# Kernel tuning notes

Hardware: AMD Instinct MI355X
Metric: run time of the kernel (lower is better)

## Reference

```python
import jax, jax.numpy as jnp
import numpy as np

B, S, D = 1, 2048, 2048      # batch, seq, hidden_dim
DF = 768                      # moe intermediate (per routed expert)
DSH = 2048                    # shared-expert intermediate
E, K = 32, 8                  # num routed experts, top_k
BLK = 128                     # fp8 block-scale size
CAP = 1024
T = B * S


def _dequant(w, s, blk=BLK):
    # w: [E, M, N] fp8 values (stored fp32), s: [E, M/blk, N/blk] block scales
    Eh, M, N = w.shape
    Mb, Nb = s.shape[1], s.shape[2]
    return (w.reshape(Eh, Mb, blk, Nb, blk) * s[:, :, None, :, None]).reshape(Eh, M, N)


def setup_inputs() -> dict:
    key = jax.random.key(0)
    ks = jax.random.split(key, 13)
    n = lambda k, shp, sc=0.02: jax.random.normal(k, shp, jnp.float32) * sc
    u = lambda k, shp: jax.random.uniform(k, shp, jnp.float32, 0.005, 0.02)
    return {
        "hidden_states": jax.random.normal(ks[0], (B, S, D), jnp.float32),
        "router_w": n(ks[1], (E, D)),
        # raw fp8-value weights (simulated as fp32 integers-in-range values) + block scale_inv
        "wg_fp8": jax.random.normal(ks[2], (E, DF, D), jnp.float32),
        "sg": u(ks[3], (E, DF // BLK, D // BLK)),
        "wu_fp8": jax.random.normal(ks[4], (E, DF, D), jnp.float32),
        "su": u(ks[5], (E, DF // BLK, D // BLK)),
        "wd_fp8": jax.random.normal(ks[6], (E, D, DF), jnp.float32),
        "sd": u(ks[7], (E, D // BLK, DF // BLK)),
        "ws_gate": n(ks[8], (DSH, D)),
        "ws_up": n(ks[9], (DSH, D)),
        "ws_down": n(ks[10], (D, DSH)),
        "w_shared_gate": n(ks[11], (1, D)),
    }


def reference(hidden_states, router_w, wg_fp8, sg, wu_fp8, su, wd_fp8, sd,
              ws_gate, ws_up, ws_down, w_shared_gate):
    x = hidden_states.reshape(-1, D)  # [T, D]

    # shared expert (SwiGLU) + its sigmoid gate
    shared = (jax.nn.silu(x @ ws_gate.T) * (x @ ws_up.T)) @ ws_down.T
    sh_gate = jax.nn.sigmoid(x @ w_shared_gate.T)  # [T, 1]

    # router: softmax -> top-k -> renormalize (Qwen MoE gate)
    probs = jax.nn.softmax(x @ router_w.T, axis=-1)          # [T, E]
    rw, sel = jax.lax.top_k(probs, K)                        # [T, K]
    rw = rw / jnp.sum(rw, axis=-1, keepdims=True)

    # capacity-based dispatch (replaces the python per-expert loop; same math)
    flat_e = sel.reshape(-1)                                 # [T*K]
    oh = jax.nn.one_hot(flat_e, E, dtype=jnp.int32)
    pos = jnp.sum(jnp.cumsum(oh, axis=0) * oh, axis=-1) - 1  # position within expert
    keep = (pos < CAP)
    pos_c = jnp.minimum(pos, CAP)                            # overflow -> scratch slot CAP
    tok = jnp.arange(T * K) // K                             # owning token of each (t,k) pair

    buf = jnp.zeros((E, CAP + 1, D), x.dtype).at[flat_e, pos_c].set(x[tok])

    # block-scale dequant (fp8*scale_inv), then per-expert SwiGLU
    Wg = _dequant(wg_fp8, sg)
    Wu = _dequant(wu_fp8, su)
    Wd = _dequant(wd_fp8, sd)
    g = jnp.einsum('ecd,efd->ecf', buf, Wg)
    up = jnp.einsum('ecd,efd->ecf', buf, Wu)
    h = jax.nn.silu(g) * up
    y = jnp.einsum('ecf,edf->ecd', h, Wd)                    # [E, CAP+1, D]

    # weighted scatter-add back to tokens (index_add_ equivalent)
    y_tok = y[flat_e, pos_c]                                 # [T*K, D]
    w_tok = rw.reshape(-1) * keep.astype(x.dtype)
    out = jax.ops.segment_sum(y_tok * w_tok[:, None], tok, num_segments=T)

    out = out + sh_gate * shared
    return out.reshape(B, S, D)
```

## Files before the change

kernel.cpp:

```cpp
#include <hip/hip_runtime.h>
#include <hip/hip_bf16.h>


#define TT   2048
#define DD   2048
#define DFF  768
#define DSH  2048
#define EE   32
#define KTOP 8
#define CAP  1024

typedef _Float16 half8  __attribute__((ext_vector_type(8)));
typedef _Float16 half4v __attribute__((ext_vector_type(4)));
typedef float    f32x4  __attribute__((ext_vector_type(4)));

__global__ __launch_bounds__(256) void k_init(int* __restrict__ cnt,
                                              int* __restrict__ slot_tok) {
  int i = blockIdx.x * 256 + threadIdx.x;
  if (i < EE * CAP) slot_tok[i] = 0;
  if (i < EE) cnt[i] = 0;
}

__global__ __launch_bounds__(64) void k_router(
    const float* __restrict__ x, const float* __restrict__ rw,
    const float* __restrict__ wshg,
    _Float16* __restrict__ x_h,
    float* __restrict__ shg, int* __restrict__ cnt,
    int* __restrict__ slot_tok, float* __restrict__ slot_w,
    int* __restrict__ slot_pair, int* __restrict__ pair_pos) {
  int t = blockIdx.x;
  int lane = threadIdx.x;
  const float* xr = x + (size_t)t * DD;
  float xv[32];
#pragma unroll
  for (int j = 0; j < 32; ++j) xv[j] = xr[lane + j * 64];

#pragma unroll
  for (int j = 0; j < 32; ++j)
    x_h[(size_t)t * DD + lane + j * 64] = (_Float16)xv[j];

  __shared__ float lg[EE];
  for (int e = 0; e < EE; ++e) {
    const float* we = rw + (size_t)e * DD;
    float s = 0.f;
#pragma unroll
    for (int j = 0; j < 32; ++j) s += xv[j] * we[lane + j * 64];
#pragma unroll
    for (int off = 32; off > 0; off >>= 1) s += __shfl_down(s, off);
    if (lane == 0) lg[e] = s;
  }
  {
    float s = 0.f;
#pragma unroll
    for (int j = 0; j < 32; ++j) s += xv[j] * wshg[lane + j * 64];
#pragma unroll
    for (int off = 32; off > 0; off >>= 1) s += __shfl_down(s, off);
    if (lane == 0) shg[t] = 1.f / (1.f + expf(-s));
  }
  if (lane == 0) {
    unsigned used = 0;
    int sel[KTOP];
    float val[KTOP];
    for (int k = 0; k < KTOP; ++k) {
      float bv = -1e30f; int bi = 0;
      for (int e = 0; e < EE; ++e)
        if (!((used >> e) & 1) && lg[e] > bv) { bv = lg[e]; bi = e; }
      used |= (1u << bi);
      sel[k] = bi; val[k] = bv;
    }
    float mx = val[0], sum = 0.f;
    for (int k = 0; k < KTOP; ++k) { val[k] = expf(val[k] - mx); sum += val[k]; }
    float inv = 1.f / sum;
    for (int k = 0; k < KTOP; ++k) {
      int e = sel[k];
      int pos = atomicAdd(&cnt[e], 1);
      pair_pos[t * KTOP + k] = pos;
      if (pos < CAP) {
        slot_tok[e * CAP + pos] = t;
        slot_w[e * CAP + pos] = val[k] * inv;
        slot_pair[e * CAP + pos] = t * KTOP + k;
      }
    }
  }
}

template<bool DUAL, bool GATHER, bool DEQ, int EPI, int KDIM>
__device__ __forceinline__ void gemm_body(
    _Float16 (*sA)[8192], _Float16 (*sB)[8192],
    const _Float16* __restrict__ Ae,
    const float* __restrict__ B0e, const float* __restrict__ B1e,
    const float* __restrict__ S0e, const float* __restrict__ S1e, int sRow,
    _Float16* __restrict__ OutH, long long outBase, int ldOut,
    int ldA, int rows, int rowBase, int nBase,
    const int* __restrict__ slotBase, const float* __restrict__ slotW) {
  constexpr int BK = 64;
  constexpr int KT = KDIM / BK;
  constexpr int NF = DUAL ? 2 : 4;
  constexpr int BCH = DUAL ? 4 : 8;

  const int tid = threadIdx.x;
  const int lane = tid & 63;
  const int wave = tid >> 6;
  const int wr = wave >> 1;
  const int wc = wave & 1;

  int aByte[4];
#pragma unroll
  for (int i = 0; i < 4; ++i) {
    int c = tid + i * 256;
    int row = c >> 3;
    int colB = ((c & 7) << 4) ^ ((row & 7) << 4);
    int src = GATHER ? slotBase[rowBase + row] : (rowBase + row);
    aByte[i] = src * (2 * ldA) + colB;
  }
  int bOff[BCH], wByte[BCH];
#pragma unroll
  for (int i = 0; i < BCH; ++i) {
    int c = tid + i * 256;
    int rn = c >> 4;
    int c4 = (c & 15) << 2;
    bOff[i] = (nBase + rn) * KDIM + c4;
    wByte[i] = ((rn << 7) + (c4 << 1)) ^ ((rn & 7) << 4);
  }

  f32x4 accG[4][NF];
  f32x4 accU[DUAL ? 4 : 1][NF];
#pragma unroll
  for (int m = 0; m < 4; ++m)
#pragma unroll
    for (int n = 0; n < NF; ++n) {
      accG[m][n] = (f32x4){0.f, 0.f, 0.f, 0.f};
      if constexpr (DUAL) accU[m][n] = (f32x4){0.f, 0.f, 0.f, 0.f};
    }

  auto stageA = [&](int kt, int buf) {
#pragma unroll
    for (int i = 0; i < 4; ++i) {
      __builtin_amdgcn_global_load_lds(
          (const __attribute__((address_space(1))) void*)
              ((const char*)Ae + aByte[i] + kt * (BK * 2)),
          (__attribute__((address_space(3))) void*)&sA[buf][(tid + i * 256) * 8],
          16, 0, 0);
    }
  };
  auto loadB = [&](int kt, float4 (&r0)[BCH], float4 (&r1)[BCH]) {
    const int ko = kt * BK;
#pragma unroll
    for (int i = 0; i < BCH; ++i) r0[i] = *(const float4*)(B0e + bOff[i] + ko);
    if constexpr (DUAL) {
#pragma unroll
      for (int i = 0; i < BCH; ++i) r1[i] = *(const float4*)(B1e + bOff[i] + ko);
    }
  };
  auto storeB = [&](int kt, float4 (&r0)[BCH], float4 (&r1)[BCH]) {
    float s0 = 1.f, s1 = 1.f;
    if constexpr (DEQ) {
      s0 = S0e[sRow + (kt >> 1)];
      if constexpr (DUAL) s1 = S1e[sRow + (kt >> 1)];
    }
    char* base = (char*)&sB[kt & 1][0];
#pragma unroll
    for (int i = 0; i < BCH; ++i) {
      half4v h = { (_Float16)(r0[i].x * s0), (_Float16)(r0[i].y * s0),
                   (_Float16)(r0[i].z * s0), (_Float16)(r0[i].w * s0) };
      *(half4v*)(base + wByte[i]) = h;
      if constexpr (DUAL) {
        half4v h1 = { (_Float16)(r1[i].x * s1), (_Float16)(r1[i].y * s1),
                      (_Float16)(r1[i].z * s1), (_Float16)(r1[i].w * s1) };
        *(half4v*)(base + 8192 + wByte[i]) = h1;
      }
    }
  };
  auto computeTile = [&](int ia, int ib) {
    const char* pA = (const char*)&sA[ia][0];
    const char* pB = (const char*)&sB[ib][0];
#pragma unroll
    for (int kk = 0; kk < 2; ++kk) {
      const int koff = kk * 32 + (lane >> 4) * 8;
      half8 a[4];
#pragma unroll
      for (int m = 0; m < 4; ++m) {
        int r = wr * 64 + m * 16 + (lane & 15);
        int byt = ((r << 7) + (koff << 1)) ^ ((r & 7) << 4);
        a[m] = *(const half8*)(pA + byt);
      }
      if constexpr (DUAL) {
        half8 bg[2], bu[2];
#pragma unroll
        for (int n = 0; n < 2; ++n) {
          int rn = wc * 32 + n * 16 + (lane & 15);
          int byt = ((rn << 7) + (koff << 1)) ^ ((rn & 7) << 4);
          bg[n] = *(const half8*)(pB + byt);
          bu[n] = *(const half8*)(pB + 8192 + byt);
        }
#pragma unroll
        for (int m = 0; m < 4; ++m)
#pragma unroll
          for (int n = 0; n < 2; ++n) {
            accG[m][n] = __builtin_amdgcn_mfma_f32_16x16x32_f16(a[m], bg[n], accG[m][n], 0, 0, 0);
            accU[m][n] = __builtin_amdgcn_mfma_f32_16x16x32_f16(a[m], bu[n], accU[m][n], 0, 0, 0);
          }
      } else {
        half8 b[4];
#pragma unroll
        for (int n = 0; n < 4; ++n) {
          int rn = wc * 64 + n * 16 + (lane & 15);
          int byt = ((rn << 7) + (koff << 1)) ^ ((rn & 7) << 4);
          b[n] = *(const half8*)(pB + byt);
        }
#pragma unroll
        for (int m = 0; m < 4; ++m)
#pragma unroll
          for (int n = 0; n < 4; ++n)
            accG[m][n] = __builtin_amdgcn_mfma_f32_16x16x32_f16(a[m], b[n], accG[m][n], 0, 0, 0);
      }
    }
  };

  float4 rbE0[BCH], rbE1[BCH], rbO0[BCH], rbO1[BCH];

  stageA(0, 0); loadB(0, rbE0, rbE1);
  __builtin_amdgcn_sched_barrier(0);
  stageA(1, 1); loadB(1, rbO0, rbO1);
  __builtin_amdgcn_sched_barrier(0);

  int bufC = 0;
  int bufW = 2;

  for (int kt = 0; kt < KT; kt += 2) {
    if (kt + 1 < KT) { asm volatile("s_waitcnt vmcnt(12)" ::: "memory"); }
    else             { asm volatile("s_waitcnt vmcnt(0)"  ::: "memory"); }
    __builtin_amdgcn_sched_barrier(0);
    storeB(kt, rbE0, rbE1);
    asm volatile("s_waitcnt lgkmcnt(0)" ::: "memory");
    __builtin_amdgcn_sched_barrier(0);
    __builtin_amdgcn_s_barrier();
    __builtin_amdgcn_sched_barrier(0);
    if (kt + 2 < KT) { stageA(kt + 2, bufW); loadB(kt + 2, rbE0, rbE1); }
    __builtin_amdgcn_sched_barrier(0);
    computeTile(bufC, 0);
    bufC = (bufC == 2) ? 0 : bufC + 1;
    bufW = (bufW == 2) ? 0 : bufW + 1;

    if (kt + 2 < KT) { asm volatile("s_waitcnt vmcnt(12)" ::: "memory"); }
    else             { asm volatile("s_waitcnt vmcnt(0)"  ::: "memory"); }
    __builtin_amdgcn_sched_barrier(0);
    storeB(kt + 1, rbO0, rbO1);
    asm volatile("s_waitcnt lgkmcnt(0)" ::: "memory");
    __builtin_amdgcn_sched_barrier(0);
    __builtin_amdgcn_s_barrier();
    __builtin_amdgcn_sched_barrier(0);
    if (kt + 3 < KT) { stageA(kt + 3, bufW); loadB(kt + 3, rbO0, rbO1); }
    __builtin_amdgcn_sched_barrier(0);
    computeTile(bufC, 1);
    bufC = (bufC == 2) ? 0 : bufC + 1;
    bufW = (bufW == 2) ? 0 : bufW + 1;
  }

#pragma unroll
  for (int m = 0; m < 4; ++m) {
#pragma unroll
    for (int i = 0; i < 4; ++i) {
      int row = rowBase + wr * 64 + m * 16 + (lane >> 4) * 4 + i;
      if (row < rows) {
        if constexpr (EPI == 1) {
          int pair = slotBase[row];
          float w = slotW[row];
#pragma unroll
          for (int n = 0; n < NF; ++n) {
            int col = nBase + wc * 64 + n * 16 + (lane & 15);
            OutH[(long long)pair * DD + col] = (_Float16)(w * accG[m][n][i]);
          }
        } else {
#pragma unroll
          for (int n = 0; n < NF; ++n) {
            int col = nBase + (DUAL ? wc * 32 : wc * 64) + n * 16 + (lane & 15);
            long long o = outBase + (long long)row * ldOut + col;
            if constexpr (DUAL) {
              float gv = accG[m][n][i];
              float uv = accU[m][n][i];
              OutH[o] = (_Float16)((gv / (1.f + __expf(-gv))) * uv);
            } else {
              OutH[o] = (_Float16)accG[m][n][i];
            }
          }
        }
      }
    }
  }
}

__global__ __launch_bounds__(256, 2) void k_gu(
    const _Float16* __restrict__ x_h,
    const float* __restrict__ wg, const float* __restrict__ wu,
    const float* __restrict__ sg, const float* __restrict__ su,
    _Float16* __restrict__ H,
    const float* __restrict__ wsg, const float* __restrict__ wsu,
    _Float16* __restrict__ Hsh,
    const int* __restrict__ cnt, const int* __restrict__ slot_tok) {
  __shared__ __align__(16) _Float16 sA[3][8192];
  __shared__ __align__(16) _Float16 sB[2][8192];
  const int bid = blockIdx.x;
  if (bid < 3072) {
    const int xcd = bid & 7, t0 = bid >> 3;
    const int mb = t0 % 8, pp = t0 / 8;
    const int p = pp * 8 + xcd;
    const int nb = p % 12, e = p / 12;
    int rows = cnt[e] > CAP ? CAP : cnt[e];
    const int rowBase = mb * 128;
    if (rowBase >= rows) return;
    gemm_body<true, true, true, 0, DD>(
        sA, sB, x_h,
        wg + (long long)e * DFF * DD, wu + (long long)e * DFF * DD,
        sg + (long long)e * ((DFF / 128) * (DD / 128)),
        su + (long long)e * ((DFF / 128) * (DD / 128)),
        ((nb * 64) >> 7) * (DD / 128),
        H, (long long)e * CAP * DFF, DFF,
        DD, rows, rowBase, nb * 64,
        slot_tok + e * CAP, nullptr);
  } else {
    const int f = bid - 3072;
    const int xcd = f & 7, t0 = f >> 3;
    const int mb = t0 % 16, pp = t0 / 16;
    const int nb = pp * 8 + xcd;
    gemm_body<true, false, false, 0, DD>(
        sA, sB, x_h,
        wsg, wsu, nullptr, nullptr, 0,
        Hsh, 0LL, DSH,
        DD, TT, mb * 128, nb * 64,
        nullptr, nullptr);
  }
}

__global__ __launch_bounds__(256, 2) void k_dn(
    const _Float16* __restrict__ H,
    const float* __restrict__ wd, const float* __restrict__ sd,
    _Float16* __restrict__ Yp,
    const _Float16* __restrict__ Hsh, const float* __restrict__ wsd,
    _Float16* __restrict__ Ysh,
    const int* __restrict__ cnt,
    const int* __restrict__ slot_pair, const float* __restrict__ slot_w) {
  __shared__ __align__(16) _Float16 sA[3][8192];
  __shared__ __align__(16) _Float16 sB[2][8192];
  const int bid = blockIdx.x;
  if (bid < 4096) {
    const int xcd = bid & 7, t0 = bid >> 3;
    const int mb = t0 % 8, pp = t0 / 8;
    const int p = pp * 8 + xcd;
    const int nb = p % 16, e = p / 16;
    int rows = cnt[e] > CAP ? CAP : cnt[e];
    const int rowBase = mb * 128;
    if (rowBase >= rows) return;
    gemm_body<false, false, true, 1, DFF>(
        sA, sB, H + (long long)e * CAP * DFF,
        wd + (long long)e * DD * DFF, wd + (long long)e * DD * DFF,
        sd + (long long)e * ((DD / 128) * (DFF / 128)), nullptr,
        ((nb * 128) >> 7) * (DFF / 128),
        Yp, 0LL, DD,
        DFF, rows, rowBase, nb * 128,
        slot_pair + e * CAP, slot_w + e * CAP);
  } else {
    const int f = bid - 4096;
    const int xcd = f & 7, t0 = f >> 3;
    const int mb = t0 % 16, pp = t0 / 16;
    const int nb = pp * 8 + xcd;
    gemm_body<false, false, false, 0, DSH>(
        sA, sB, Hsh,
        wsd, wsd, nullptr, nullptr, 0,
        Ysh, 0LL, DD,
        DSH, TT, mb * 128, nb * 128,
        nullptr, nullptr);
  }
}

__global__ __launch_bounds__(256) void k_combine2(
    const _Float16* __restrict__ Yp, const _Float16* __restrict__ Ysh,
    const float* __restrict__ shg, const int* __restrict__ pair_pos,
    float* __restrict__ out) {
  int t = blockIdx.x;
  int col = threadIdx.x * 8;
  float acc[8];
  half8 ys = *(const half8*)&Ysh[(size_t)t * DD + col];
  float g = shg[t];
#pragma unroll
  for (int j = 0; j < 8; ++j) acc[j] = g * (float)ys[j];
#pragma unroll
  for (int k = 0; k < KTOP; ++k) {
    if (pair_pos[t * KTOP + k] < CAP) {
      half8 y = *(const half8*)&Yp[((size_t)t * KTOP + k) * DD + col];
#pragma unroll
      for (int j = 0; j < 8; ++j) acc[j] += (float)y[j];
    }
  }
  float4 o0 = {acc[0], acc[1], acc[2], acc[3]};
  float4 o1 = {acc[4], acc[5], acc[6], acc[7]};
  *(float4*)&out[(size_t)t * DD + col] = o0;
  *(float4*)&out[(size_t)t * DD + col + 4] = o1;
}

extern "C" void kernel_launch(void* const* d_in, const int* in_sizes, int n_in,
                              void* d_out, int out_size, void* d_ws, size_t ws_size,
                              hipStream_t stream) {
  (void)in_sizes; (void)n_in; (void)out_size; (void)ws_size;
  const float* x    = (const float*)d_in[0];
  const float* rw   = (const float*)d_in[1];
  const float* wg   = (const float*)d_in[2];
  const float* sg   = (const float*)d_in[3];
  const float* wu   = (const float*)d_in[4];
  const float* su   = (const float*)d_in[5];
  const float* wd   = (const float*)d_in[6];
  const float* sd   = (const float*)d_in[7];
  const float* wsg  = (const float*)d_in[8];
  const float* wsu  = (const float*)d_in[9];
  const float* wsd  = (const float*)d_in[10];
  const float* wshg = (const float*)d_in[11];
  float* out = (float*)d_out;

  char* p = (char*)d_ws;
  auto alloc = [&](size_t bytes) {
    char* r = p;
    p += (bytes + 255) & ~(size_t)255;
    return r;
  };
  _Float16* x_h   = (_Float16*)alloc((size_t)TT * DD * 2);
  _Float16* H     = (_Float16*)alloc((size_t)EE * CAP * DFF * 2);
  _Float16* Hsh   = (_Float16*)alloc((size_t)TT * DSH * 2);
  _Float16* Yp    = (_Float16*)alloc((size_t)TT * KTOP * DD * 2);
  _Float16* Ysh   = (_Float16*)alloc((size_t)TT * DD * 2);
  float* shg      = (float*)alloc((size_t)TT * 4);
  int* cnt        = (int*)alloc((size_t)EE * 4);
  int* slot_tok   = (int*)alloc((size_t)EE * CAP * 4);
  float* slot_w   = (float*)alloc((size_t)EE * CAP * 4);
  int* slot_pair  = (int*)alloc((size_t)EE * CAP * 4);
  int* pair_pos   = (int*)alloc((size_t)TT * KTOP * 4);

  k_init<<<(EE * CAP + 255) / 256, 256, 0, stream>>>(cnt, slot_tok);
  k_router<<<TT, 64, 0, stream>>>(x, rw, wshg, x_h, shg, cnt, slot_tok,
                                  slot_w, slot_pair, pair_pos);

  k_gu<<<3584, 256, 0, stream>>>(x_h, wg, wu, sg, su, H, wsg, wsu, Hsh,
                                 cnt, slot_tok);

  k_dn<<<4352, 256, 0, stream>>>(H, wd, sd, Yp, Hsh, wsd, Ysh,
                                 cnt, slot_pair, slot_w);

  k_combine2<<<TT, 256, 0, stream>>>(Yp, Ysh, shg, pair_pos, out);
}
```

Measured before the change: 655.0 us.

## Pre-convert shared-expert weights to fp16 and use direct-to-LDS GEMM path

```diff
diff --git a/kernel.cpp b/kernel.cpp
--- a/kernel.cpp
+++ b/kernel.cpp
@@ -24,7 +24,9 @@
 __global__ __launch_bounds__(64) void k_router(
     const float* __restrict__ x, const float* __restrict__ rw,
     const float* __restrict__ wshg,
+    const float* __restrict__ wsg, const float* __restrict__ wsu,
     _Float16* __restrict__ x_h,
+    _Float16* __restrict__ wsg_h, _Float16* __restrict__ wsu_h,
     float* __restrict__ shg, int* __restrict__ cnt,
     int* __restrict__ slot_tok, float* __restrict__ slot_w,
     int* __restrict__ slot_pair, int* __restrict__ pair_pos) {
@@ -80,6 +82,22 @@
         slot_w[e * CAP + pos] = val[k] * inv;
         slot_pair[e * CAP + pos] = t * KTOP + k;
       }
+    }
+  }
+
+  {
+    const int gtid = t * 64 + lane;
+    const float4* s0 = (const float4*)wsg;
+    const float4* s1 = (const float4*)wsu;
+#pragma unroll
+    for (int i = 0; i < 8; ++i) {
+      int idx = gtid + i * 131072;
+      float4 v = s0[idx];
+      ((half4v*)wsg_h)[idx] = (half4v){(_Float16)v.x, (_Float16)v.y,
+                                       (_Float16)v.z, (_Float16)v.w};
+      float4 w = s1[idx];
+      ((half4v*)wsu_h)[idx] = (half4v){(_Float16)w.x, (_Float16)w.y,
+                                       (_Float16)w.z, (_Float16)w.w};
     }
   }
 }
@@ -224,8 +242,7 @@
   stageA(1, 1); loadB(1, rbO0, rbO1);
   __builtin_amdgcn_sched_barrier(0);
 
-  int bufC = 0;
-  int bufW = 2;
+  int bufC = 0, bufW = 2;
 
   for (int kt = 0; kt < KT; kt += 2) {
     if (kt + 1 < KT) { asm volatile("s_waitcnt vmcnt(12)" ::: "memory"); }
@@ -290,17 +307,191 @@
   }
 }
 
+template<bool DUAL, int KDIM>
+__device__ __forceinline__ void gemm_body16(
+    _Float16 (*sA)[8192], _Float16 (*sB)[8192],
+    const _Float16* __restrict__ Ae,
+    const _Float16* __restrict__ B0e, const _Float16* __restrict__ B1e,
+    _Float16* __restrict__ OutH, int ldOut,
+    int ldA, int rows, int rowBase, int nBase) {
+  constexpr int KT = KDIM / 64;
+  constexpr int NF = DUAL ? 2 : 4;
+
+  const int tid = threadIdx.x;
+  const int lane = tid & 63;
+  const int wave = tid >> 6;
+  const int wr = wave >> 1;
+  const int wc = wave & 1;
+
+  int aByte[4];
+#pragma unroll
+  for (int i = 0; i < 4; ++i) {
+    int c = tid + i * 256;
+    int row = c >> 3;
+    int colB = ((c & 7) << 4) ^ ((row & 7) << 4);
+    aByte[i] = (rowBase + row) * (2 * ldA) + colB;
+  }
+  int bByte[4];
+#pragma unroll
+  for (int i = 0; i < 4; ++i) {
+    int c = tid + i * 256;
+    int rn = DUAL ? ((c & 511) >> 3) : (c >> 3);
+    int colB = ((c & 7) << 4) ^ ((rn & 7) << 4);
+    bByte[i] = (nBase + rn) * (2 * KDIM) + colB;
+  }
+
+  f32x4 accG[4][NF];
+  f32x4 accU[DUAL ? 4 : 1][NF];
+#pragma unroll
+  for (int m = 0; m < 4; ++m)
+#pragma unroll
+    for (int n = 0; n < NF; ++n) {
+      accG[m][n] = (f32x4){0.f, 0.f, 0.f, 0.f};
+      if constexpr (DUAL) accU[m][n] = (f32x4){0.f, 0.f, 0.f, 0.f};
+    }
+
+  auto stageA = [&](int kt, int buf) {
+#pragma unroll
+    for (int i = 0; i < 4; ++i) {
+      __builtin_amdgcn_global_load_lds(
+          (const __attribute__((address_space(1))) void*)
+              ((const char*)Ae + aByte[i] + kt * 128),
+          (__attribute__((address_space(3))) void*)&sA[buf][(tid + i * 256) * 8],
+          16, 0, 0);
+    }
+  };
+  auto stageB = [&](int kt, int buf) {
+#pragma unroll
+    for (int i = 0; i < 4; ++i) {
+      const _Float16* src = (DUAL && i >= 2) ? B1e : B0e;
+      __builtin_amdgcn_global_load_lds(
+          (const __attribute__((address_space(1))) void*)
+              ((const char*)src + bByte[i] + kt * 128),
+          (__attribute__((address_space(3))) void*)&sB[buf][(tid + i * 256) * 8],
+          16, 0, 0);
+    }
+  };
+  auto computeTile = [&](int ia, int ib) {
+    const char* pA = (const char*)&sA[ia][0];
+    const char* pB = (const char*)&sB[ib][0];
+#pragma unroll
+    for (int kk = 0; kk < 2; ++kk) {
+      const int koff = kk * 32 + (lane >> 4) * 8;
+      half8 a[4];
+#pragma unroll
+      for (int m = 0; m < 4; ++m) {
+        int r = wr * 64 + m * 16 + (lane & 15);
+        int byt = ((r << 7) + (koff << 1)) ^ ((r & 7) << 4);
+        a[m] = *(const half8*)(pA + byt);
+      }
+      if constexpr (DUAL) {
+        half8 bg[2], bu[2];
+#pragma unroll
+        for (int n = 0; n < 2; ++n) {
+          int rn = wc * 32 + n * 16 + (lane & 15);
+          int byt = ((rn << 7) + (koff << 1)) ^ ((rn & 7) << 4);
+          bg[n] = *(const half8*)(pB + byt);
+          bu[n] = *(const half8*)(pB + 8192 + byt);
+        }
+#pragma unroll
+        for (int m = 0; m < 4; ++m)
+#pragma unroll
+          for (int n = 0; n < 2; ++n) {
+            accG[m][n] = __builtin_amdgcn_mfma_f32_16x16x32_f16(a[m], bg[n], accG[m][n], 0, 0, 0);
+            accU[m][n] = __builtin_amdgcn_mfma_f32_16x16x32_f16(a[m], bu[n], accU[m][n], 0, 0, 0);
+          }
+      } else {
+        half8 b[4];
+#pragma unroll
+        for (int n = 0; n < 4; ++n) {
+          int rn = wc * 64 + n * 16 + (lane & 15);
+          int byt = ((rn << 7) + (koff << 1)) ^ ((rn & 7) << 4);
+          b[n] = *(const half8*)(pB + byt);
+        }
+#pragma unroll
+        for (int m = 0; m < 4; ++m)
+#pragma unroll
+          for (int n = 0; n < 4; ++n)
+            accG[m][n] = __builtin_amdgcn_mfma_f32_16x16x32_f16(a[m], b[n], accG[m][n], 0, 0, 0);
+      }
+    }
+  };
+
+  stageB(0, 0);
+  __builtin_amdgcn_sched_barrier(0);
+  stageA(0, 0);
+  __builtin_amdgcn_sched_barrier(0);
+  stageA(1, 1);
+  __builtin_amdgcn_sched_barrier(0);
+
+  int bufC = 0, bufW = 2;
+  for (int kt = 0; kt < KT; ++kt) {
+    asm volatile("s_waitcnt lgkmcnt(0)" ::: "memory");
+    if (kt + 1 < KT) { asm volatile("s_waitcnt vmcnt(4)" ::: "memory"); }
+    else             { asm volatile("s_waitcnt vmcnt(0)" ::: "memory"); }
+    __builtin_amdgcn_sched_barrier(0);
+    __builtin_amdgcn_s_barrier();
+    __builtin_amdgcn_sched_barrier(0);
+    if (kt + 1 < KT) stageB(kt + 1, (kt + 1) & 1);
+    if (kt + 2 < KT) stageA(kt + 2, bufW);
+    __builtin_amdgcn_sched_barrier(0);
+    computeTile(bufC, kt & 1);
+    bufC = (bufC == 2) ? 0 : bufC + 1;
+    bufW = (bufW == 2) ? 0 : bufW + 1;
+  }
+
+#pragma unroll
+  for (int m = 0; m < 4; ++m) {
+#pragma unroll
+    for (int i = 0; i < 4; ++i) {
+      int row = rowBase + wr * 64 + m * 16 + (lane >> 4) * 4 + i;
+      if (row < rows) {
+#pragma unroll
+        for (int n = 0; n < NF; ++n) {
+          int col = nBase + (DUAL ? wc * 32 : wc * 64) + n * 16 + (lane & 15);
+          long long o = (long long)row * ldOut + col;
+          if constexpr (DUAL) {
+            float gv = accG[m][n][i];
+            float uv = accU[m][n][i];
+            OutH[o] = (_Float16)((gv / (1.f + __expf(-gv))) * uv);
+          } else {
+            OutH[o] = (_Float16)accG[m][n][i];
+          }
+        }
+      }
+    }
+  }
+}
+
 __global__ __launch_bounds__(256, 2) void k_gu(
     const _Float16* __restrict__ x_h,
     const float* __restrict__ wg, const float* __restrict__ wu,
     const float* __restrict__ sg, const float* __restrict__ su,
     _Float16* __restrict__ H,
-    const float* __restrict__ wsg, const float* __restrict__ wsu,
+    const _Float16* __restrict__ wsg_h, const _Float16* __restrict__ wsu_h,
     _Float16* __restrict__ Hsh,
+    const float* __restrict__ wsd, _Float16* __restrict__ wsd_h,
     const int* __restrict__ cnt, const int* __restrict__ slot_tok) {
   __shared__ __align__(16) _Float16 sA[3][8192];
   __shared__ __align__(16) _Float16 sB[2][8192];
   const int bid = blockIdx.x;
+  const int tid = threadIdx.x;
+
+  {
+    const int tot4 = DD * DSH / 4;
+    int base = bid * 293;
+#pragma unroll
+    for (int j = 0; j < 2; ++j) {
+      int off = tid + j * 256;
+      int idx = base + off;
+      if (off < 293 && idx < tot4) {
+        float4 v = ((const float4*)wsd)[idx];
+        ((half4v*)wsd_h)[idx] = (half4v){(_Float16)v.x, (_Float16)v.y,
+                                         (_Float16)v.z, (_Float16)v.w};
+      }
+    }
+  }
+
   if (bid < 3072) {
     const int xcd = bid & 7, t0 = bid >> 3;
     const int mb = t0 % 8, pp = t0 / 8;
@@ -323,12 +514,9 @@
     const int xcd = f & 7, t0 = f >> 3;
     const int mb = t0 % 16, pp = t0 / 16;
     const int nb = pp * 8 + xcd;
-    gemm_body<true, false, false, 0, DD>(
-        sA, sB, x_h,
-        wsg, wsu, nullptr, nullptr, 0,
-        Hsh, 0LL, DSH,
-        DD, TT, mb * 128, nb * 64,
-        nullptr, nullptr);
+    gemm_body16<true, DD>(
+        sA, sB, x_h, wsg_h, wsu_h,
+        Hsh, DSH, DD, TT, mb * 128, nb * 64);
   }
 }
 
@@ -336,7 +524,7 @@
     const _Float16* __restrict__ H,
     const float* __restrict__ wd, const float* __restrict__ sd,
     _Float16* __restrict__ Yp,
-    const _Float16* __restrict__ Hsh, const float* __restrict__ wsd,
+    const _Float16* __restrict__ Hsh, const _Float16* __restrict__ wsd_h,
     _Float16* __restrict__ Ysh,
     const int* __restrict__ cnt,
     const int* __restrict__ slot_pair, const float* __restrict__ slot_w) {
@@ -364,12 +552,9 @@
     const int xcd = f & 7, t0 = f >> 3;
     const int mb = t0 % 16, pp = t0 / 16;
     const int nb = pp * 8 + xcd;
-    gemm_body<false, false, false, 0, DSH>(
-        sA, sB, Hsh,
-        wsd, wsd, nullptr, nullptr, 0,
-        Ysh, 0LL, DD,
-        DSH, TT, mb * 128, nb * 128,
-        nullptr, nullptr);
+    gemm_body16<false, DSH>(
+        sA, sB, Hsh, wsd_h, wsd_h,
+        Ysh, DD, DSH, TT, mb * 128, nb * 128);
   }
 }
 
@@ -427,6 +612,9 @@
   _Float16* Hsh   = (_Float16*)alloc((size_t)TT * DSH * 2);
   _Float16* Yp    = (_Float16*)alloc((size_t)TT * KTOP * DD * 2);
   _Float16* Ysh   = (_Float16*)alloc((size_t)TT * DD * 2);
+  _Float16* wsg_h = (_Float16*)alloc((size_t)DSH * DD * 2);
+  _Float16* wsu_h = (_Float16*)alloc((size_t)DSH * DD * 2);
+  _Float16* wsd_h = (_Float16*)alloc((size_t)DD * DSH * 2);
   float* shg      = (float*)alloc((size_t)TT * 4);
   int* cnt        = (int*)alloc((size_t)EE * 4);
   int* slot_tok   = (int*)alloc((size_t)EE * CAP * 4);
@@ -435,13 +623,14 @@
   int* pair_pos   = (int*)alloc((size_t)TT * KTOP * 4);
 
   k_init<<<(EE * CAP + 255) / 256, 256, 0, stream>>>(cnt, slot_tok);
-  k_router<<<TT, 64, 0, stream>>>(x, rw, wshg, x_h, shg, cnt, slot_tok,
-                                  slot_w, slot_pair, pair_pos);
-
-  k_gu<<<3584, 256, 0, stream>>>(x_h, wg, wu, sg, su, H, wsg, wsu, Hsh,
-                                 cnt, slot_tok);
-
-  k_dn<<<4352, 256, 0, stream>>>(H, wd, sd, Yp, Hsh, wsd, Ysh,
+  k_router<<<TT, 64, 0, stream>>>(x, rw, wshg, wsg, wsu, x_h, wsg_h, wsu_h,
+                                  shg, cnt, slot_tok, slot_w,
+                                  slot_pair, pair_pos);
+
+  k_gu<<<3584, 256, 0, stream>>>(x_h, wg, wu, sg, su, H, wsg_h, wsu_h, Hsh,
+                                 wsd, wsd_h, cnt, slot_tok);
+
+  k_dn<<<4352, 256, 0, stream>>>(H, wd, sd, Yp, Hsh, wsd_h, Ysh,
                                  cnt, slot_pair, slot_w);
 
   k_combine2<<<TT, 256, 0, stream>>>(Yp, Ysh, shg, pair_pos, out);
```

New measurement: 656.2 us. Within noise of the previous version (+0.2%).
